# Performance work log

Measured on AMD Instinct MI355X. Metric: run time of the kernel, lower is better.

## Reference

```python
import jax, jax.numpy as jnp
import numpy as np
import math

B, T, C = 2, 2048, 1024
N_HEAD = 16
D_HEAD = C // N_HEAD


def setup_inputs() -> dict:
    key = jax.random.key(0)
    k1, k2, k3, k4, k5 = jax.random.split(key, 5)
    # weights stored as [in, out] (transpose of torch Linear.weight) so y = x @ W + b
    return {
        "x": jax.random.normal(k1, (B, T, C), dtype=jnp.float32),
        "w_qkv": jax.random.normal(k2, (C, 3 * C), dtype=jnp.float32) * (1.0 / math.sqrt(C)),
        "b_qkv": jax.random.normal(k3, (3 * C,), dtype=jnp.float32) * 0.01,
        "w_proj": jax.random.normal(k4, (C, C), dtype=jnp.float32) * (1.0 / math.sqrt(C)),
        "b_proj": jax.random.normal(k5, (C,), dtype=jnp.float32) * 0.01,
    }


def reference(x, w_qkv, b_qkv, w_proj, b_proj):
    b, t, c = x.shape
    n_head, d_head = N_HEAD, c // N_HEAD
    qkv = x @ w_qkv + b_qkv                      # [b, t, 3c]
    q, k, v = jnp.split(qkv, 3, axis=-1)         # each [b, t, c]

    def to_heads(a):
        return a.reshape(b, t, n_head, d_head).transpose(0, 2, 1, 3)  # [b,h,t,d]

    q, k, v = to_heads(q), to_heads(k), to_heads(v)
    scale = 1.0 / math.sqrt(d_head)
    # non-causal naive attention: full [b,h,t,t] scores
    w = jnp.einsum("bhtd,bhsd->bhts", q, k) * scale
    w = jax.nn.softmax(w, axis=-1)
    o = jnp.einsum("bhts,bhsd->bhtd", w, v)      # [b,h,t,d]
    o = o.transpose(0, 2, 1, 3).reshape(b, t, c)  # [b,t,c]
    return o @ w_proj + b_proj
```

## Files before the change

kernel.cpp:

```cpp
#include <hip/hip_runtime.h>
#include <hip/hip_bf16.h>

typedef __attribute__((ext_vector_type(8))) short bf16x8;
typedef __attribute__((ext_vector_type(4))) float f32x4;
typedef __attribute__((ext_vector_type(4))) unsigned int u32x4;

static constexpr int BB = 2, T = 2048, C = 1024, NH = 16, DH = 64;

__device__ __forceinline__ void gload16(const void* g, void* l) {
  __builtin_amdgcn_global_load_lds(
      (const __attribute__((address_space(1))) unsigned int*)g,
      (__attribute__((address_space(3))) unsigned int*)l, 16, 0, 0);
}

__device__ __forceinline__ unsigned pack_bf16(float lo, float hi) {
  unsigned a = (unsigned)__bfloat16_as_ushort(__float2bfloat16(lo));
  unsigned b = (unsigned)__bfloat16_as_ushort(__float2bfloat16(hi));
  return a | (b << 16);
}

__device__ __forceinline__ float fast_exp2(float x) {
#if __has_builtin(__builtin_amdgcn_exp2f)
  return __builtin_amdgcn_exp2f(x);
#else
  return exp2f(x);
#endif
}

__global__ __launch_bounds__(256) void k_prep(const float* __restrict__ x,
                                              __hip_bfloat16* __restrict__ xb,
                                              const float* __restrict__ wq,
                                              __hip_bfloat16* __restrict__ wqt,
                                              const float* __restrict__ wp,
                                              __hip_bfloat16* __restrict__ wpt) {
  __shared__ float tile[32][33];
  const int bid = blockIdx.x, tid = threadIdx.x;
  if (bid < 4096) {
    const int i = bid * 256 + tid;
    float4 v = reinterpret_cast<const float4*>(x)[i];
    __hip_bfloat16 h[4];
    h[0] = __float2bfloat16(v.x); h[1] = __float2bfloat16(v.y);
    h[2] = __float2bfloat16(v.z); h[3] = __float2bfloat16(v.w);
    reinterpret_cast<uint2*>(xb)[i] = *reinterpret_cast<uint2*>(h);
    return;
  }
  const float* in;
  __hip_bfloat16* out;
  int K, N, bx, by;
  if (bid < 7168) {
    const int b2 = bid - 4096;
    in = wq; out = wqt; K = 1024; N = 3072; bx = b2 % 96; by = b2 / 96;
  } else {
    const int b2 = bid - 7168;
    in = wp; out = wpt; K = 1024; N = 1024; bx = b2 % 32; by = b2 / 32;
  }
  const int n0 = bx * 32, k0 = by * 32;
  const int tx = tid & 31, ty = tid >> 5;
#pragma unroll
  for (int i = 0; i < 32; i += 8)
    tile[ty + i][tx] = in[(size_t)(k0 + ty + i) * N + n0 + tx];
  __syncthreads();
#pragma unroll
  for (int i = 0; i < 32; i += 8)
    out[(size_t)(n0 + ty + i) * K + k0 + tx] = __float2bfloat16(tile[tx][ty + i]);
}

__global__ __launch_bounds__(256, 2) void k_gemmqkv(
    const __hip_bfloat16* __restrict__ A, const __hip_bfloat16* __restrict__ Bt,
    const float* __restrict__ bias,
    __hip_bfloat16* __restrict__ oq, __hip_bfloat16* __restrict__ okk,
    __hip_bfloat16* __restrict__ ovt) {
  __shared__ __align__(16) char smem[65536];
  const int tid = threadIdx.x;
  const int w = tid >> 6, lane = tid & 63;
  const int lr = lane & 15, lg = lane >> 4;
  const int wm = (w >> 1) * 64, wn = (w & 1) * 64;
  const int m0 = blockIdx.x * 128, n0 = blockIdx.y * 128;

  const int scol = (((tid & 7) ^ ((tid >> 3) & 7)) << 4);
  const char* Ag = (const char*)A + (size_t)(m0 + (tid >> 3)) * 2048 + scol;
  const char* Bg = (const char*)Bt + (size_t)(n0 + (tid >> 3)) * 2048 + scol;
  const size_t ldst = (size_t)(tid & ~63) * 16;

  auto stage = [&](int ks, char* lA) {
    const char* ag = Ag + (size_t)ks * 128;
    const char* bg = Bg + (size_t)ks * 128;
    char* lB = lA + 16384;
#pragma unroll
    for (int j = 0; j < 4; ++j) {
      gload16(ag + (size_t)j * 65536, lA + j * 4096 + ldst);
      gload16(bg + (size_t)j * 65536, lB + j * 4096 + ldst);
    }
  };

  const int swz = (lr & 7) << 4;
  const int aofs = (wm + lr) * 128;
  const int bofs = 16384 + (wn + lr) * 128;
  const int x0 = (lg * 16) ^ swz;
  const int x1 = (64 + lg * 16) ^ swz;
  const char* A00 = smem + aofs + x0;
  const char* A01 = smem + aofs + x1;
  const char* B00 = smem + bofs + x0;
  const char* B01 = smem + bofs + x1;
  const char* A10 = A00 + 32768;
  const char* A11 = A01 + 32768;
  const char* B10 = B00 + 32768;
  const char* B11 = B01 + 32768;

  f32x4 acc[4][4] = {};

  auto compute = [&](const char* pA0, const char* pA1, const char* pB0,
                     const char* pB1) {
#pragma unroll
    for (int kk = 0; kk < 2; ++kk) {
      const char* pA = kk ? pA1 : pA0;
      const char* pB = kk ? pB1 : pB0;
      bf16x8 a[4], b[4];
#pragma unroll
      for (int mi = 0; mi < 4; ++mi)
        a[mi] = *reinterpret_cast<const bf16x8*>(pA + mi * 2048);
#pragma unroll
      for (int ni = 0; ni < 4; ++ni)
        b[ni] = *reinterpret_cast<const bf16x8*>(pB + ni * 2048);
      __builtin_amdgcn_s_setprio(1);
#pragma unroll
      for (int mi = 0; mi < 4; ++mi)
#pragma unroll
        for (int ni = 0; ni < 4; ++ni)
          acc[mi][ni] =
              __builtin_amdgcn_mfma_f32_16x16x32_bf16(a[mi], b[ni], acc[mi][ni], 0, 0, 0);
      __builtin_amdgcn_s_setprio(0);
    }
  };

  stage(0, smem);
  __syncthreads();
  for (int it = 0; it < 8; ++it) {
    stage(2 * it + 1, smem + 32768);
    compute(A00, A01, B00, B01);
    __syncthreads();
    if (it < 7) stage(2 * it + 2, smem);
    compute(A10, A11, B10, B11);
    __syncthreads();
  }

  const int region = n0 >> 10;
  float bias_r[4];
#pragma unroll
  for (int ni = 0; ni < 4; ++ni) bias_r[ni] = bias[n0 + wn + ni * 16 + lr];

  if (region < 2) {
    __hip_bfloat16* dst = (region == 0) ? oq : okk;
    const float sc = (region == 0) ? 0.1803368801111244f : 1.0f;
#pragma unroll
    for (int mi = 0; mi < 4; ++mi) {
#pragma unroll
      for (int ni = 0; ni < 4; ++ni) {
        const int nn = n0 + wn + ni * 16 + lr;
        const int cc = nn & 1023, h = cc >> 6, d = cc & 63;
#pragma unroll
        for (int r = 0; r < 4; ++r) {
          const int m = m0 + wm + mi * 16 + lg * 4 + r;
          const int bb = m >> 11, t = m & 2047;
          dst[((size_t)(bb * NH + h) * T + t) * DH + d] =
              __float2bfloat16((acc[mi][ni][r] + bias_r[ni]) * sc);
        }
      }
    }
  } else {
    char* E = smem + w * 8192;
#pragma unroll
    for (int mi = 0; mi < 4; ++mi) {
      const int mlb = mi * 16 + lg * 4;
      const int mp = (mlb & 35) | ((mlb & 12) << 1) | ((mlb & 16) >> 2);
#pragma unroll
      for (int ni = 0; ni < 4; ++ni) {
        const int dl = ni * 16 + lr;
        const int rs = (dl & 7) << 4;
        const unsigned v01 = pack_bf16(acc[mi][ni][0] + bias_r[ni],
                                       acc[mi][ni][1] + bias_r[ni]);
        const unsigned v23 = pack_bf16(acc[mi][ni][2] + bias_r[ni],
                                       acc[mi][ni][3] + bias_r[ni]);
        *reinterpret_cast<unsigned*>(&E[dl * 128 + ((mp * 2) ^ rs)]) = v01;
        *reinterpret_cast<unsigned*>(&E[dl * 128 + (((mp + 2) * 2) ^ rs)]) = v23;
      }
    }
    const int hh = ((n0 + wn) & 1023) >> 6;
    const int bb = m0 >> 11, tb = (m0 & 2047) + wm;
    __hip_bfloat16* dst = ovt + ((size_t)(bb * NH + hh) * DH) * T + tb;
    const int lrs = (lane & 7) << 4;
#pragma unroll
    for (int j = 0; j < 8; ++j) {
      u32x4 v = *reinterpret_cast<const u32x4*>(&E[lane * 128 + ((j * 16) ^ lrs)]);
      *reinterpret_cast<u32x4*>(&dst[(size_t)lane * T + j * 8]) = v;
    }
  }
}

__global__ __launch_bounds__(256, 2) void k_gemmproj(
    const __hip_bfloat16* __restrict__ A, const __hip_bfloat16* __restrict__ Bt,
    const float* __restrict__ bias, float* __restrict__ of) {
  constexpr int N = 1024;
  __shared__ __align__(16) char smem[65536];
  const int tid = threadIdx.x;
  const int w = tid >> 6, lane = tid & 63;
  const int lr = lane & 15, lg = lane >> 4;
  const int wm = (w >> 1) * 64, wn = (w & 1) * 64;
  const int m0 = blockIdx.x * 128, n0 = blockIdx.y * 128;

  const int scol = (((tid & 7) ^ ((tid >> 3) & 7)) << 4);
  const char* Ag = (const char*)A + (size_t)(m0 + (tid >> 3)) * 2048 + scol;
  const char* Bg = (const char*)Bt + (size_t)(n0 + (tid >> 3)) * 2048 + scol;
  const size_t ldst = (size_t)(tid & ~63) * 16;

  auto stage = [&](int ks, char* lA) {
    const char* ag = Ag + (size_t)ks * 128;
    const char* bg = Bg + (size_t)ks * 128;
    char* lB = lA + 16384;
#pragma unroll
    for (int j = 0; j < 4; ++j) {
      gload16(ag + (size_t)j * 65536, lA + j * 4096 + ldst);
      gload16(bg + (size_t)j * 65536, lB + j * 4096 + ldst);
    }
  };

  const int swz = (lr & 7) << 4;
  const int aofs = (wm + lr) * 128;
  const int bofs = 16384 + (wn + lr) * 128;
  const int x0 = (lg * 16) ^ swz;
  const int x1 = (64 + lg * 16) ^ swz;
  const char* A00 = smem + aofs + x0;
  const char* A01 = smem + aofs + x1;
  const char* B00 = smem + bofs + x0;
  const char* B01 = smem + bofs + x1;
  const char* A10 = A00 + 32768;
  const char* A11 = A01 + 32768;
  const char* B10 = B00 + 32768;
  const char* B11 = B01 + 32768;

  f32x4 acc[4][4] = {};

  auto compute = [&](const char* pA0, const char* pA1, const char* pB0,
                     const char* pB1) {
#pragma unroll
    for (int kk = 0; kk < 2; ++kk) {
      const char* pA = kk ? pA1 : pA0;
      const char* pB = kk ? pB1 : pB0;
      bf16x8 a[4], b[4];
#pragma unroll
      for (int mi = 0; mi < 4; ++mi)
        a[mi] = *reinterpret_cast<const bf16x8*>(pA + mi * 2048);
#pragma unroll
      for (int ni = 0; ni < 4; ++ni)
        b[ni] = *reinterpret_cast<const bf16x8*>(pB + ni * 2048);
      __builtin_amdgcn_s_setprio(1);
#pragma unroll
      for (int mi = 0; mi < 4; ++mi)
#pragma unroll
        for (int ni = 0; ni < 4; ++ni)
          acc[mi][ni] =
              __builtin_amdgcn_mfma_f32_16x16x32_bf16(a[mi], b[ni], acc[mi][ni], 0, 0, 0);
      __builtin_amdgcn_s_setprio(0);
    }
  };

  stage(0, smem);
  __syncthreads();
  for (int it = 0; it < 8; ++it) {
    stage(2 * it + 1, smem + 32768);
    compute(A00, A01, B00, B01);
    __syncthreads();
    if (it < 7) stage(2 * it + 2, smem);
    compute(A10, A11, B10, B11);
    __syncthreads();
  }

  float bias_r[4];
#pragma unroll
  for (int ni = 0; ni < 4; ++ni) bias_r[ni] = bias[n0 + wn + ni * 16 + lr];

#pragma unroll
  for (int mi = 0; mi < 4; ++mi)
#pragma unroll
    for (int ni = 0; ni < 4; ++ni) {
      const int n = n0 + wn + ni * 16 + lr;
#pragma unroll
      for (int r = 0; r < 4; ++r) {
        const int m = m0 + wm + mi * 16 + lg * 4 + r;
        of[(size_t)m * N + n] = acc[mi][ni][r] + bias_r[ni];
      }
    }
}

__global__ __launch_bounds__(256, 4) void k_attn(const __hip_bfloat16* __restrict__ Q,
                                                 const __hip_bfloat16* __restrict__ Kc,
                                                 const __hip_bfloat16* __restrict__ Vt,
                                                 __hip_bfloat16* __restrict__ O) {
  __shared__ __align__(16) char smem[2][16384];
  const int tid = threadIdx.x;
  const int w = tid >> 6, lane = tid & 63;
  const int lr = lane & 15, lg = lane >> 4;
  const int n = blockIdx.x;
  const int xtile = (n >> 3) & 31;
  const int bh = ((n >> 8) << 3) | (n & 7);
  const int b = bh >> 4, h = bh & 15;
  const int t0 = xtile * 64 + w * 16;
  const __hip_bfloat16* Qh = Q + (size_t)bh * T * DH;
  const char* Kbase = (const char*)(Kc + (size_t)bh * T * DH);
  const char* Vbase = (const char*)(Vt + (size_t)bh * DH * T);

  const int srow = tid >> 3;
  const int scol = (((tid & 7) ^ (srow & 7)) << 4);
  const size_t ldst = (size_t)(tid & ~63) * 16;
  const char* Kg = Kbase + (size_t)srow * 128 + scol;
  const char* Vg = Vbase + (size_t)srow * 4096 + scol;

  const int swz = (lr & 7) << 4;
  const int lbA = lr * 128 + ((lg * 16) ^ swz);
  const int lbB = lr * 128 + ((64 + lg * 16) ^ swz);
  const char* kA0 = smem[0] + lbA;
  const char* kB0 = smem[0] + lbB;
  const char* kA1 = smem[1] + lbA;
  const char* kB1 = smem[1] + lbB;

  auto stage = [&](int kv, char* kb, char* vb) {
    const char* kg = Kg + (size_t)kv * 128;
    const char* vg = Vg + (size_t)kv * 2;
    gload16(kg, kb + ldst);
    gload16(kg + 4096, kb + 4096 + ldst);
    gload16(vg, vb + ldst);
    gload16(vg + 131072, vb + 4096 + ldst);
  };

  bf16x8 q[2];
#pragma unroll
  for (int kf = 0; kf < 2; ++kf)
    q[kf] = *reinterpret_cast<const bf16x8*>(&Qh[(size_t)(t0 + lr) * DH + kf * 32 + lg * 8]);

  f32x4 o[4] = {};
  float lsum = 0.f;

  auto compute = [&](const char* kA, const char* kB) {
    bf16x8 bk[4][2];
#pragma unroll
    for (int nj = 0; nj < 4; ++nj) {
      bk[nj][0] = *reinterpret_cast<const bf16x8*>(kA + nj * 2048);
      bk[nj][1] = *reinterpret_cast<const bf16x8*>(kB + nj * 2048);
    }

    f32x4 s[4] = {};
    __builtin_amdgcn_s_setprio(1);
#pragma unroll
    for (int nj = 0; nj < 4; ++nj) {
      s[nj] = __builtin_amdgcn_mfma_f32_16x16x32_bf16(bk[nj][0], q[0], s[nj], 0, 0, 0);
      s[nj] = __builtin_amdgcn_mfma_f32_16x16x32_bf16(bk[nj][1], q[1], s[nj], 0, 0, 0);
    }
    __builtin_amdgcn_s_setprio(0);

    bf16x8 av[4][2];
#pragma unroll
    for (int nd = 0; nd < 4; ++nd) {
      av[nd][0] = *reinterpret_cast<const bf16x8*>(kA + 8192 + nd * 2048);
      av[nd][1] = *reinterpret_cast<const bf16x8*>(kB + 8192 + nd * 2048);
    }

#pragma unroll
    for (int nj = 0; nj < 4; ++nj)
#pragma unroll
      for (int r = 0; r < 4; ++r) s[nj][r] = fast_exp2(s[nj][r]);
    {
      float a0 = (s[0][0] + s[0][1]) + (s[0][2] + s[0][3]);
      float a1 = (s[1][0] + s[1][1]) + (s[1][2] + s[1][3]);
      float a2 = (s[2][0] + s[2][1]) + (s[2][2] + s[2][3]);
      float a3 = (s[3][0] + s[3][1]) + (s[3][2] + s[3][3]);
      lsum += (a0 + a1) + (a2 + a3);
    }

    bf16x8 pa[2];
#pragma unroll
    for (int c = 0; c < 2; ++c) {
      u32x4 pw;
      pw[0] = pack_bf16(s[2 * c][0], s[2 * c][1]);
      pw[1] = pack_bf16(s[2 * c][2], s[2 * c][3]);
      pw[2] = pack_bf16(s[2 * c + 1][0], s[2 * c + 1][1]);
      pw[3] = pack_bf16(s[2 * c + 1][2], s[2 * c + 1][3]);
      pa[c] = __builtin_bit_cast(bf16x8, pw);
    }

    __builtin_amdgcn_s_setprio(1);
#pragma unroll
    for (int nd = 0; nd < 4; ++nd)
#pragma unroll
      for (int c = 0; c < 2; ++c)
        o[nd] = __builtin_amdgcn_mfma_f32_16x16x32_bf16(av[nd][c], pa[c], o[nd], 0, 0, 0);
    __builtin_amdgcn_s_setprio(0);
  };

  stage(0, smem[0], smem[0] + 8192);
  __syncthreads();

  for (int it = 0; it < 15; ++it) {
    const int kv = it * 128;
    stage(kv + 64, smem[1], smem[1] + 8192);
    compute(kA0, kB0);
    __syncthreads();
    stage(kv + 128, smem[0], smem[0] + 8192);
    compute(kA1, kB1);
    __syncthreads();
  }
  stage(1984, smem[1], smem[1] + 8192);
  compute(kA0, kB0);
  __syncthreads();
  compute(kA1, kB1);

  lsum += __shfl_xor(lsum, 16);
  lsum += __shfl_xor(lsum, 32);
  const float inv = 1.0f / lsum;

#pragma unroll
  for (int nd = 0; nd < 4; ++nd) {
    uint2 st;
    st.x = pack_bf16(o[nd][0] * inv, o[nd][1] * inv);
    st.y = pack_bf16(o[nd][2] * inv, o[nd][3] * inv);
    *reinterpret_cast<uint2*>(
        &O[(size_t)(b * T + t0 + lr) * C + h * DH + nd * 16 + lg * 4]) = st;
  }
}

extern "C" void kernel_launch(void* const* d_in, const int* in_sizes, int n_in,
                              void* d_out, int out_size, void* d_ws, size_t ws_size,
                              hipStream_t stream) {
  const float* x      = (const float*)d_in[0];
  const float* w_qkv  = (const float*)d_in[1];
  const float* b_qkv  = (const float*)d_in[2];
  const float* w_proj = (const float*)d_in[3];
  const float* b_proj = (const float*)d_in[4];
  float* out = (float*)d_out;

  __hip_bfloat16* ws  = (__hip_bfloat16*)d_ws;
  __hip_bfloat16* xb  = ws;
  __hip_bfloat16* wqt = xb + 4194304;
  __hip_bfloat16* wpt = wqt + 3145728;
  __hip_bfloat16* Qb  = wpt + 1048576;
  __hip_bfloat16* Kb  = Qb + 4194304;
  __hip_bfloat16* Vtb = Kb + 4194304;
  __hip_bfloat16* Ob  = Vtb + 4194304;

  k_prep<<<8192, 256, 0, stream>>>(x, xb, w_qkv, wqt, w_proj, wpt);
  k_gemmqkv<<<dim3(32, 24), 256, 0, stream>>>(xb, wqt, b_qkv, Qb, Kb, Vtb);
  k_attn<<<1024, 256, 0, stream>>>(Qb, Kb, Vtb, Ob);
  k_gemmproj<<<dim3(32, 8), 256, 0, stream>>>(Ob, wpt, b_proj, out);
}
```

Baseline: 108.3 us.

## Process two query tiles per wave in attention to reuse K/V fragments

Each wave now handles 32 query rows instead of 16, so every K and V fragment loaded from shared memory feeds two MFMA chains. The block covers 128 queries, which halves the grid to 512 blocks and halves the total K/V global-to-LDS traffic. In exchange, register pressure roughly doubles, so launch bounds drop to 2 blocks per SM, and with fewer blocks some compute units may sit idle.

```diff
diff --git a/kernel.cpp b/kernel.cpp
--- a/kernel.cpp
+++ b/kernel.cpp
@@ -292,7 +292,7 @@
     }
 }
 
-__global__ __launch_bounds__(256, 4) void k_attn(const __hip_bfloat16* __restrict__ Q,
+__global__ __launch_bounds__(256, 2) void k_attn(const __hip_bfloat16* __restrict__ Q,
                                                  const __hip_bfloat16* __restrict__ Kc,
                                                  const __hip_bfloat16* __restrict__ Vt,
                                                  __hip_bfloat16* __restrict__ O) {
@@ -301,10 +301,10 @@
   const int w = tid >> 6, lane = tid & 63;
   const int lr = lane & 15, lg = lane >> 4;
   const int n = blockIdx.x;
-  const int xtile = (n >> 3) & 31;
-  const int bh = ((n >> 8) << 3) | (n & 7);
+  const int xtile = (n >> 3) & 15;
+  const int bh = ((n >> 7) << 3) | (n & 7);
   const int b = bh >> 4, h = bh & 15;
-  const int t0 = xtile * 64 + w * 16;
+  const int t0 = xtile * 128 + w * 32;
   const __hip_bfloat16* Qh = Q + (size_t)bh * T * DH;
   const char* Kbase = (const char*)(Kc + (size_t)bh * T * DH);
   const char* Vbase = (const char*)(Vt + (size_t)bh * DH * T);
@@ -332,13 +332,15 @@
     gload16(vg + 131072, vb + 4096 + ldst);
   };
 
-  bf16x8 q[2];
-#pragma unroll
-  for (int kf = 0; kf < 2; ++kf)
-    q[kf] = *reinterpret_cast<const bf16x8*>(&Qh[(size_t)(t0 + lr) * DH + kf * 32 + lg * 8]);
-
-  f32x4 o[4] = {};
-  float lsum = 0.f;
+  bf16x8 q0[2], q1[2];
+#pragma unroll
+  for (int kf = 0; kf < 2; ++kf) {
+    q0[kf] = *reinterpret_cast<const bf16x8*>(&Qh[(size_t)(t0 + lr) * DH + kf * 32 + lg * 8]);
+    q1[kf] = *reinterpret_cast<const bf16x8*>(&Qh[(size_t)(t0 + 16 + lr) * DH + kf * 32 + lg * 8]);
+  }
+
+  f32x4 o0[4] = {}, o1[4] = {};
+  float l0 = 0.f, l1 = 0.f;
 
   auto compute = [&](const char* kA, const char* kB) {
     bf16x8 bk[4][2];
@@ -348,12 +350,14 @@
       bk[nj][1] = *reinterpret_cast<const bf16x8*>(kB + nj * 2048);
     }
 
-    f32x4 s[4] = {};
+    f32x4 s0[4] = {}, s1[4] = {};
     __builtin_amdgcn_s_setprio(1);
 #pragma unroll
     for (int nj = 0; nj < 4; ++nj) {
-      s[nj] = __builtin_amdgcn_mfma_f32_16x16x32_bf16(bk[nj][0], q[0], s[nj], 0, 0, 0);
-      s[nj] = __builtin_amdgcn_mfma_f32_16x16x32_bf16(bk[nj][1], q[1], s[nj], 0, 0, 0);
+      s0[nj] = __builtin_amdgcn_mfma_f32_16x16x32_bf16(bk[nj][0], q0[0], s0[nj], 0, 0, 0);
+      s0[nj] = __builtin_amdgcn_mfma_f32_16x16x32_bf16(bk[nj][1], q0[1], s0[nj], 0, 0, 0);
+      s1[nj] = __builtin_amdgcn_mfma_f32_16x16x32_bf16(bk[nj][0], q1[0], s1[nj], 0, 0, 0);
+      s1[nj] = __builtin_amdgcn_mfma_f32_16x16x32_bf16(bk[nj][1], q1[1], s1[nj], 0, 0, 0);
     }
     __builtin_amdgcn_s_setprio(0);
 
@@ -367,32 +371,47 @@
 #pragma unroll
     for (int nj = 0; nj < 4; ++nj)
 #pragma unroll
-      for (int r = 0; r < 4; ++r) s[nj][r] = fast_exp2(s[nj][r]);
+      for (int r = 0; r < 4; ++r) {
+        s0[nj][r] = fast_exp2(s0[nj][r]);
+        s1[nj][r] = fast_exp2(s1[nj][r]);
+      }
     {
-      float a0 = (s[0][0] + s[0][1]) + (s[0][2] + s[0][3]);
-      float a1 = (s[1][0] + s[1][1]) + (s[1][2] + s[1][3]);
-      float a2 = (s[2][0] + s[2][1]) + (s[2][2] + s[2][3]);
-      float a3 = (s[3][0] + s[3][1]) + (s[3][2] + s[3][3]);
-      lsum += (a0 + a1) + (a2 + a3);
-    }
-
-    bf16x8 pa[2];
+      float a0 = (s0[0][0] + s0[0][1]) + (s0[0][2] + s0[0][3]);
+      float a1 = (s0[1][0] + s0[1][1]) + (s0[1][2] + s0[1][3]);
+      float a2 = (s0[2][0] + s0[2][1]) + (s0[2][2] + s0[2][3]);
+      float a3 = (s0[3][0] + s0[3][1]) + (s0[3][2] + s0[3][3]);
+      l0 += (a0 + a1) + (a2 + a3);
+      float b0 = (s1[0][0] + s1[0][1]) + (s1[0][2] + s1[0][3]);
+      float b1 = (s1[1][0] + s1[1][1]) + (s1[1][2] + s1[1][3]);
+      float b2 = (s1[2][0] + s1[2][1]) + (s1[2][2] + s1[2][3]);
+      float b3 = (s1[3][0] + s1[3][1]) + (s1[3][2] + s1[3][3]);
+      l1 += (b0 + b1) + (b2 + b3);
+    }
+
+    bf16x8 pa0[2], pa1[2];
 #pragma unroll
     for (int c = 0; c < 2; ++c) {
-      u32x4 pw;
-      pw[0] = pack_bf16(s[2 * c][0], s[2 * c][1]);
-      pw[1] = pack_bf16(s[2 * c][2], s[2 * c][3]);
-      pw[2] = pack_bf16(s[2 * c + 1][0], s[2 * c + 1][1]);
-      pw[3] = pack_bf16(s[2 * c + 1][2], s[2 * c + 1][3]);
-      pa[c] = __builtin_bit_cast(bf16x8, pw);
+      u32x4 w0, w1;
+      w0[0] = pack_bf16(s0[2 * c][0], s0[2 * c][1]);
+      w0[1] = pack_bf16(s0[2 * c][2], s0[2 * c][3]);
+      w0[2] = pack_bf16(s0[2 * c + 1][0], s0[2 * c + 1][1]);
+      w0[3] = pack_bf16(s0[2 * c + 1][2], s0[2 * c + 1][3]);
+      pa0[c] = __builtin_bit_cast(bf16x8, w0);
+      w1[0] = pack_bf16(s1[2 * c][0], s1[2 * c][1]);
+      w1[1] = pack_bf16(s1[2 * c][2], s1[2 * c][3]);
+      w1[2] = pack_bf16(s1[2 * c + 1][0], s1[2 * c + 1][1]);
+      w1[3] = pack_bf16(s1[2 * c + 1][2], s1[2 * c + 1][3]);
+      pa1[c] = __builtin_bit_cast(bf16x8, w1);
     }
 
     __builtin_amdgcn_s_setprio(1);
 #pragma unroll
     for (int nd = 0; nd < 4; ++nd)
 #pragma unroll
-      for (int c = 0; c < 2; ++c)
-        o[nd] = __builtin_amdgcn_mfma_f32_16x16x32_bf16(av[nd][c], pa[c], o[nd], 0, 0, 0);
+      for (int c = 0; c < 2; ++c) {
+        o0[nd] = __builtin_amdgcn_mfma_f32_16x16x32_bf16(av[nd][c], pa0[c], o0[nd], 0, 0, 0);
+        o1[nd] = __builtin_amdgcn_mfma_f32_16x16x32_bf16(av[nd][c], pa1[c], o1[nd], 0, 0, 0);
+      }
     __builtin_amdgcn_s_setprio(0);
   };
 
@@ -413,17 +432,21 @@
   __syncthreads();
   compute(kA1, kB1);
 
-  lsum += __shfl_xor(lsum, 16);
-  lsum += __shfl_xor(lsum, 32);
-  const float inv = 1.0f / lsum;
+  l0 += __shfl_xor(l0, 16); l0 += __shfl_xor(l0, 32);
+  l1 += __shfl_xor(l1, 16); l1 += __shfl_xor(l1, 32);
+  const float inv0 = 1.0f / l0, inv1 = 1.0f / l1;
 
 #pragma unroll
   for (int nd = 0; nd < 4; ++nd) {
     uint2 st;
-    st.x = pack_bf16(o[nd][0] * inv, o[nd][1] * inv);
-    st.y = pack_bf16(o[nd][2] * inv, o[nd][3] * inv);
+    st.x = pack_bf16(o0[nd][0] * inv0, o0[nd][1] * inv0);
+    st.y = pack_bf16(o0[nd][2] * inv0, o0[nd][3] * inv0);
     *reinterpret_cast<uint2*>(
         &O[(size_t)(b * T + t0 + lr) * C + h * DH + nd * 16 + lg * 4]) = st;
+    st.x = pack_bf16(o1[nd][0] * inv1, o1[nd][1] * inv1);
+    st.y = pack_bf16(o1[nd][2] * inv1, o1[nd][3] * inv1);
+    *reinterpret_cast<uint2*>(
+        &O[(size_t)(b * T + t0 + 16 + lr) * C + h * DH + nd * 16 + lg * 4]) = st;
   }
 }
 
@@ -448,6 +471,6 @@
 
   k_prep<<<8192, 256, 0, stream>>>(x, xb, w_qkv, wqt, w_proj, wpt);
   k_gemmqkv<<<dim3(32, 24), 256, 0, stream>>>(xb, wqt, b_qkv, Qb, Kb, Vtb);
-  k_attn<<<1024, 256, 0, stream>>>(Qb, Kb, Vtb, Ob);
+  k_attn<<<512, 256, 0, stream>>>(Qb, Kb, Vtb, Ob);
   k_gemmproj<<<dim3(32, 8), 256, 0, stream>>>(Ob, wpt, b_proj, out);
 }
```

Result: faster. 102.3 us (median of 2 runs) (-5.6%).
